# Performance work log

Measured on AMD Instinct MI355X. Metric: run time of the kernel, lower is better.

Reference implementation:

```python
import jax, jax.numpy as jnp
import numpy as np
import math

B, S, H, NH, K = 1, 4096, 1024, 16, 32
HD = H // NH


def setup_inputs() -> dict:
    key = jax.random.key(0)
    ks = jax.random.split(key, 8)
    x = jax.random.normal(ks[0], (B, S, H), dtype=jnp.float32)
    # per-query top-K indices; make them causal (idx[q] <= q) so every row has >=1 valid key
    idx_raw = jax.random.randint(ks[1], (S, K), 0, S)
    idx = idx_raw % (jnp.arange(S)[:, None] + 1)
    valid = jnp.ones((S, K), dtype=bool)
    geo_bias = jax.random.normal(ks[2], (NH, S, K), dtype=jnp.float32)
    scale = 1.0 / math.sqrt(H)
    Wq = jax.random.normal(ks[3], (H, H), dtype=jnp.float32) * scale
    Wk = jax.random.normal(ks[4], (H, H), dtype=jnp.float32) * scale
    Wv = jax.random.normal(ks[5], (H, H), dtype=jnp.float32) * scale
    Wo = jax.random.normal(ks[6], (H, H), dtype=jnp.float32) * scale
    bo = jnp.zeros((H,), dtype=jnp.float32)
    return {"x": x, "idx": idx, "valid": valid, "geo_bias": geo_bias,
            "Wq": Wq, "Wk": Wk, "Wv": Wv, "Wo": Wo, "bo": bo}


def reference(x, idx, valid, geo_bias, Wq, Wk, Wv, Wo, bo):
    b, s, h = x.shape
    nh = geo_bias.shape[0]
    hd = h // nh
    kk = idx.shape[1]
    # projections -> [b, nh, s, hd]
    def proj(W):
        return (x @ W).reshape(b, s, nh, hd).transpose(0, 2, 1, 3)
    q, k, v = proj(Wq), proj(Wk), proj(Wv)
    # gather per-query selected keys/values: [b, nh, s, K, hd]
    k_sel = k[:, :, idx]
    v_sel = v[:, :, idx]
    # scores via elementwise mult + reduce over head_dim
    logits = jnp.einsum('bhsd,bhskd->bhsk', q, k_sel) / math.sqrt(hd)
    logits = logits + geo_bias[None]
    mask = valid & (idx <= jnp.arange(s)[:, None])  # [s, K]
    logits = jnp.where(mask[None, None], logits, jnp.float32(-1e30))
    attn = jax.nn.softmax(logits, axis=-1)
    out = jnp.einsum('bhsk,bhskd->bhsd', attn, v_sel)
    out = out.transpose(0, 2, 1, 3).reshape(b, s, h)
    return out @ Wo + bo
```

## Files before the change

### kernel.cpp

```cpp
#include <hip/hip_runtime.h>
#include <hip/hip_bf16.h>
#include <stdint.h>

typedef unsigned short u16;
typedef __attribute__((ext_vector_type(8))) short bf16x8;
typedef __attribute__((ext_vector_type(4))) float f32x4;
typedef __attribute__((ext_vector_type(2))) float f32x2;

typedef const __attribute__((address_space(1))) unsigned int* gptr_t;
typedef __attribute__((address_space(3))) unsigned int* lptr_t;

__device__ __forceinline__ float bf2f(u16 v) {
    unsigned int u = ((unsigned int)v) << 16;
    float f;
    __builtin_memcpy(&f, &u, 4);
    return f;
}
__device__ __forceinline__ u16 f2bf(float f) {
    unsigned int u;
    __builtin_memcpy(&u, &f, 4);
    u += 0x7FFFu + ((u >> 16) & 1u);
    return (u16)(u >> 16);
}
__device__ __forceinline__ float bflo(unsigned int u) {
    unsigned int x = u << 16; float f; __builtin_memcpy(&f, &x, 4); return f;
}
__device__ __forceinline__ float bfhi(unsigned int u) {
    unsigned int x = u & 0xFFFF0000u; float f; __builtin_memcpy(&f, &x, 4); return f;
}
__device__ __forceinline__ f32x2 upk(unsigned int u) {
    return (f32x2){bflo(u), bfhi(u)};
}

#define BM 128
#define BN 128
#define BK 32

template <typename OUTT>
__global__ __launch_bounds__(256) void gemm_bt(const u16* __restrict__ A,
                                               const u16* __restrict__ Bt,
                                               OUTT* __restrict__ C,
                                               const float* __restrict__ bias,
                                               int M, int N, int K) {
    __shared__ u16 As[BM * BK];
    __shared__ u16 Bs[BN * BK];

    const int t    = threadIdx.x;
    const int lane = t & 63;
    const int wave = t >> 6;
    const int wm   = (wave >> 1) * 64;
    const int wn   = (wave & 1) * 64;
    const int m0   = blockIdx.y * BM;
    const int n0   = blockIdx.x * BN;

    const int row  = t >> 2;
    const int kcol = (t & 3) * 8;

    const int quad = lane >> 4;
    const int l16  = lane & 15;

    f32x4 acc[4][4];
#pragma unroll
    for (int i = 0; i < 4; i++)
#pragma unroll
        for (int j = 0; j < 4; j++) acc[i][j] = (f32x4){0.f, 0.f, 0.f, 0.f};

    for (int k0 = 0; k0 < K; k0 += BK) {
        const u16* ga  = A  + (size_t)(m0 + row) * K + k0 + kcol;
        const u16* ga2 = A  + (size_t)(m0 + 64 + row) * K + k0 + kcol;
        const u16* gb  = Bt + (size_t)(n0 + row) * K + k0 + kcol;
        const u16* gb2 = Bt + (size_t)(n0 + 64 + row) * K + k0 + kcol;
        __builtin_amdgcn_global_load_lds((gptr_t)ga,  (lptr_t)(&As[t * 8]),        16, 0, 0);
        __builtin_amdgcn_global_load_lds((gptr_t)ga2, (lptr_t)(&As[2048 + t * 8]), 16, 0, 0);
        __builtin_amdgcn_global_load_lds((gptr_t)gb,  (lptr_t)(&Bs[t * 8]),        16, 0, 0);
        __builtin_amdgcn_global_load_lds((gptr_t)gb2, (lptr_t)(&Bs[2048 + t * 8]), 16, 0, 0);
        __syncthreads();

        bf16x8 af[4], bfg[4];
#pragma unroll
        for (int i = 0; i < 4; i++)
            af[i] = *(const bf16x8*)&As[(wm + i * 16 + l16) * BK + quad * 8];
#pragma unroll
        for (int j = 0; j < 4; j++)
            bfg[j] = *(const bf16x8*)&Bs[(wn + j * 16 + l16) * BK + quad * 8];

#pragma unroll
        for (int i = 0; i < 4; i++)
#pragma unroll
            for (int j = 0; j < 4; j++)
                acc[i][j] = __builtin_amdgcn_mfma_f32_16x16x32_bf16(af[i], bfg[j], acc[i][j], 0, 0, 0);
        __syncthreads();
    }

#pragma unroll
    for (int j = 0; j < 4; j++) {
        const int n  = n0 + wn + j * 16 + l16;
        const float bv = bias ? bias[n] : 0.f;
#pragma unroll
        for (int i = 0; i < 4; i++) {
            const int mbase = m0 + wm + i * 16 + quad * 4;
#pragma unroll
            for (int r = 0; r < 4; r++) {
                const float v = acc[i][j][r] + bv;
                if constexpr (sizeof(OUTT) == 2)
                    C[(size_t)(mbase + r) * N + n] = (OUTT)f2bf(v);
                else
                    C[(size_t)(mbase + r) * N + n] = (OUTT)v;
            }
        }
    }
}

__global__ __launch_bounds__(512) void gemm_bt_w8(const u16* __restrict__ A,
                                                  const u16* __restrict__ Bt,
                                                  float* __restrict__ C,
                                                  const float* __restrict__ bias,
                                                  int M, int N, int K) {
    __shared__ u16 As[BM * BK];
    __shared__ u16 Bs[BN * BK];

    const int t    = threadIdx.x;
    const int lane = t & 63;
    const int wave = t >> 6;
    const int wm   = (wave >> 2) * 64;
    const int wn   = (wave & 3) * 32;
    const int m0   = blockIdx.y * BM;
    const int n0   = blockIdx.x * BN;

    const int row  = t >> 2;
    const int kcol = (t & 3) * 8;

    const int quad = lane >> 4;
    const int l16  = lane & 15;

    f32x4 acc[4][2];
#pragma unroll
    for (int i = 0; i < 4; i++)
#pragma unroll
        for (int j = 0; j < 2; j++) acc[i][j] = (f32x4){0.f, 0.f, 0.f, 0.f};

    for (int k0 = 0; k0 < K; k0 += BK) {
        const u16* ga = A  + (size_t)(m0 + row) * K + k0 + kcol;
        const u16* gb = Bt + (size_t)(n0 + row) * K + k0 + kcol;
        __builtin_amdgcn_global_load_lds((gptr_t)ga, (lptr_t)(&As[t * 8]), 16, 0, 0);
        __builtin_amdgcn_global_load_lds((gptr_t)gb, (lptr_t)(&Bs[t * 8]), 16, 0, 0);
        __syncthreads();

        bf16x8 af[4], bfg[2];
#pragma unroll
        for (int i = 0; i < 4; i++)
            af[i] = *(const bf16x8*)&As[(wm + i * 16 + l16) * BK + quad * 8];
#pragma unroll
        for (int j = 0; j < 2; j++)
            bfg[j] = *(const bf16x8*)&Bs[(wn + j * 16 + l16) * BK + quad * 8];

#pragma unroll
        for (int i = 0; i < 4; i++)
#pragma unroll
            for (int j = 0; j < 2; j++)
                acc[i][j] = __builtin_amdgcn_mfma_f32_16x16x32_bf16(af[i], bfg[j], acc[i][j], 0, 0, 0);
        __syncthreads();
    }

#pragma unroll
    for (int j = 0; j < 2; j++) {
        const int n  = n0 + wn + j * 16 + l16;
        const float bv = bias ? bias[n] : 0.f;
#pragma unroll
        for (int i = 0; i < 4; i++) {
            const int mbase = m0 + wm + i * 16 + quad * 4;
#pragma unroll
            for (int r = 0; r < 4; r++)
                C[(size_t)(mbase + r) * N + n] = acc[i][j][r] + bv;
        }
    }
}

__global__ __launch_bounds__(256) void prep_k(const float* __restrict__ x,
                                              const float* __restrict__ W0,
                                              const float* __restrict__ W1,
                                              const float* __restrict__ W2,
                                              const float* __restrict__ W3,
                                              u16* __restrict__ x_bf,
                                              u16* __restrict__ Dqkv,
                                              u16* __restrict__ Do) {
    const int b = blockIdx.x;
    if (b < 4096) {
        const int i = b * 256 + threadIdx.x;
        const float4 v = ((const float4*)x)[i];
        u16 o[4] = {f2bf(v.x), f2bf(v.y), f2bf(v.z), f2bf(v.w)};
        *(uint64_t*)&x_bf[i * 4] = *(uint64_t*)o;
        return;
    }
    __shared__ u16 tile[32][33];
    const int bb  = b - 4096;
    const int z   = bb >> 10;
    const int t10 = bb & 1023;
    const int c0  = (t10 & 31) * 32;
    const int r0  = (t10 >> 5) * 32;
    const float* src = (z == 0) ? W0 : (z == 1) ? W1 : (z == 2) ? W2 : W3;
    u16* dst = (z < 3) ? (Dqkv + (size_t)z * 1024 * 1024) : Do;
    const int tx = threadIdx.x & 31;
    const int ty = threadIdx.x >> 5;
#pragma unroll
    for (int i = 0; i < 32; i += 8)
        tile[ty + i][tx] = f2bf(src[(size_t)(r0 + ty + i) * 1024 + c0 + tx]);
    __syncthreads();
#pragma unroll
    for (int i = 0; i < 32; i += 8)
        dst[(size_t)(c0 + ty + i) * 1024 + r0 + tx] = tile[tx][ty + i];
}

__global__ __launch_bounds__(256, 8) void attn_k(const u16* __restrict__ QKV,
                                                 const int* __restrict__ idx,
                                                 const float* __restrict__ geo,
                                                 u16* __restrict__ AO) {
    __shared__ float dot_lds[4 * 64];
    __shared__ float w_lds[4 * 64];

    const int t    = threadIdx.x;
    const int lane = t & 63;
    const int wave = t >> 6;
    const int b    = blockIdx.x;
    const int hp   = b & 7;
    const int s    = ((b >> 3) << 2) + wave;
    const int h0   = hp * 2;
    const int hsel = lane >> 5;
    const int kk   = lane & 31;
    const int g    = lane >> 3;
    const int c8   = lane & 7;

    const char* qb = (const char*)QKV;

    const int j    = idx[s * 32 + kk];
    const int joff = j * 6144;

    const uint4 qA = *(const uint4*)(qb + (size_t)s * 6144 + h0 * 128 + c8 * 16);
    const uint4 qB = *(const uint4*)(qb + (size_t)s * 6144 + h0 * 128 + 128 + c8 * 16);
    const f32x2 qa0 = upk(qA.x), qa1 = upk(qA.y), qa2 = upk(qA.z), qa3 = upk(qA.w);
    const f32x2 qb0 = upk(qB.x), qb1 = upk(qB.y), qb2 = upk(qB.z), qb3 = upk(qB.w);

#pragma unroll
    for (int i = 0; i < 8; i++) {
        const int rh = i * 8 + g;
        const int jm = __shfl(j, rh & 31);
        const uint4 kv = *(const uint4*)(qb + (size_t)(unsigned)(jm * 6144) + 2048 +
                                         (h0 + (i >> 2)) * 128 + c8 * 16);
        f32x2 d2;
        if (i < 4) {
            d2  = upk(kv.x) * qa0;
            d2 += upk(kv.y) * qa1;
            d2 += upk(kv.z) * qa2;
            d2 += upk(kv.w) * qa3;
        } else {
            d2  = upk(kv.x) * qb0;
            d2 += upk(kv.y) * qb1;
            d2 += upk(kv.z) * qb2;
            d2 += upk(kv.w) * qb3;
        }
        float d = d2.x + d2.y;
        d += __shfl_xor(d, 1);
        d += __shfl_xor(d, 2);
        d += __shfl_xor(d, 4);
        if (c8 == 0) dot_lds[wave * 64 + rh] = d;
    }

    float lg2 = dot_lds[wave * 64 + lane] * 0.125f +
                geo[((size_t)(h0 + hsel) * 4096 + s) * 32 + kk];
    if (j > s) lg2 = -1e30f;

    float mx = lg2;
    mx = fmaxf(mx, __shfl_xor(mx, 16));
    mx = fmaxf(mx, __shfl_xor(mx, 8));
    mx = fmaxf(mx, __shfl_xor(mx, 4));
    mx = fmaxf(mx, __shfl_xor(mx, 2));
    mx = fmaxf(mx, __shfl_xor(mx, 1));
    const float p = __expf(lg2 - mx);
    float sum = p;
    sum += __shfl_xor(sum, 16);
    sum += __shfl_xor(sum, 8);
    sum += __shfl_xor(sum, 4);
    sum += __shfl_xor(sum, 2);
    sum += __shfl_xor(sum, 1);
    const float w = p / sum;
    w_lds[wave * 64 + lane] = w;

    const int vofs = 4096 + h0 * 128 + 4 * lane;
    f32x2 av = (f32x2){0.f, 0.f};
#pragma unroll
    for (int q = 0; q < 32; q++) {
        const int soff = __builtin_amdgcn_readlane(joff, q);
        const float wq = w_lds[wave * 64 + (lane & 32) + q];
        const unsigned int vv = *(const unsigned int*)(qb + (size_t)(unsigned)soff + vofs);
        av += wq * upk(vv);
    }
    const unsigned int packed = (unsigned int)f2bf(av.x) | ((unsigned int)f2bf(av.y) << 16);
    *(unsigned int*)&AO[(size_t)s * 1024 + h0 * 64 + 2 * lane] = packed;
}

extern "C" void kernel_launch(void* const* d_in, const int* in_sizes, int n_in,
                              void* d_out, int out_size, void* d_ws, size_t ws_size,
                              hipStream_t stream) {
    const float* x   = (const float*)d_in[0];
    const int*   idx = (const int*)d_in[1];
    const float* geo = (const float*)d_in[3];
    const float* Wq  = (const float*)d_in[4];
    const float* Wk  = (const float*)d_in[5];
    const float* Wv  = (const float*)d_in[6];
    const float* Wo  = (const float*)d_in[7];
    const float* bo  = (const float*)d_in[8];
    float* out = (float*)d_out;

    u16* x_bf   = (u16*)d_ws;
    u16* wt_qkv = x_bf + (size_t)4096 * 1024;
    u16* wt_o   = wt_qkv + (size_t)3 * 1024 * 1024;
    u16* qkv    = wt_o + (size_t)1024 * 1024;
    u16* ao     = qkv + (size_t)4096 * 3072;

    const dim3 tb(256);
    prep_k<<<dim3(8192), tb, 0, stream>>>(x, Wq, Wk, Wv, Wo, x_bf, wt_qkv, wt_o);

    gemm_bt<u16><<<dim3(3072 / BN, 4096 / BM), tb, 0, stream>>>(x_bf, wt_qkv, qkv, nullptr,
                                                                4096, 3072, 1024);
    attn_k<<<dim3(4096 * 8 / 4), tb, 0, stream>>>(qkv, idx, geo, ao);
    gemm_bt_w8<<<dim3(1024 / BN, 4096 / BM), dim3(512), 0, stream>>>(ao, wt_o, out, bo,
                                                                     4096, 1024, 1024);
}
```

Before: 188.3 us.

## Use BK=64 swizzled LDS tiles in QKV GEMM and widen attention V gather

The QKV projection GEMM now stages 64-wide K tiles in shared memory with an XOR swizzle on the 16-byte column chunks. This halves the number of barrier-separated iterations and is meant to avoid LDS bank conflicts on the fragment reads. Separately, the attention PV accumulation has each lane load 8 bytes (4 bf16) instead of 4, splits the 32 keys between the two half-waves, and combines the halves with a cross-half shuffle. The cost is more shared memory per block, which can lower occupancy, plus extra shuffles in attention.

```diff
diff --git a/kernel.cpp b/kernel.cpp
--- a/kernel.cpp
+++ b/kernel.cpp
@@ -36,14 +36,12 @@
 #define BN 128
 #define BK 32
 
-template <typename OUTT>
-__global__ __launch_bounds__(256) void gemm_bt(const u16* __restrict__ A,
-                                               const u16* __restrict__ Bt,
-                                               OUTT* __restrict__ C,
-                                               const float* __restrict__ bias,
-                                               int M, int N, int K) {
-    __shared__ u16 As[BM * BK];
-    __shared__ u16 Bs[BN * BK];
+__global__ __launch_bounds__(256) void gemm_bk64(const u16* __restrict__ A,
+                                                 const u16* __restrict__ Bt,
+                                                 u16* __restrict__ C,
+                                                 int M, int N, int K) {
+    __shared__ u16 As[BM * 64];
+    __shared__ u16 Bs[BN * 64];
 
     const int t    = threadIdx.x;
     const int lane = t & 63;
@@ -53,11 +51,13 @@
     const int m0   = blockIdx.y * BM;
     const int n0   = blockIdx.x * BN;
 
-    const int row  = t >> 2;
-    const int kcol = (t & 3) * 8;
+    const int r5   = t >> 3;
+    const int pc   = t & 7;
+    const int lc   = pc ^ (r5 & 7);
 
     const int quad = lane >> 4;
     const int l16  = lane & 15;
+    const int sw   = l16 & 7;
 
     f32x4 acc[4][4];
 #pragma unroll
@@ -65,48 +65,43 @@
 #pragma unroll
         for (int j = 0; j < 4; j++) acc[i][j] = (f32x4){0.f, 0.f, 0.f, 0.f};
 
-    for (int k0 = 0; k0 < K; k0 += BK) {
-        const u16* ga  = A  + (size_t)(m0 + row) * K + k0 + kcol;
-        const u16* ga2 = A  + (size_t)(m0 + 64 + row) * K + k0 + kcol;
-        const u16* gb  = Bt + (size_t)(n0 + row) * K + k0 + kcol;
-        const u16* gb2 = Bt + (size_t)(n0 + 64 + row) * K + k0 + kcol;
-        __builtin_amdgcn_global_load_lds((gptr_t)ga,  (lptr_t)(&As[t * 8]),        16, 0, 0);
-        __builtin_amdgcn_global_load_lds((gptr_t)ga2, (lptr_t)(&As[2048 + t * 8]), 16, 0, 0);
-        __builtin_amdgcn_global_load_lds((gptr_t)gb,  (lptr_t)(&Bs[t * 8]),        16, 0, 0);
-        __builtin_amdgcn_global_load_lds((gptr_t)gb2, (lptr_t)(&Bs[2048 + t * 8]), 16, 0, 0);
+    for (int k0 = 0; k0 < K; k0 += 64) {
+#pragma unroll
+        for (int p = 0; p < 4; p++) {
+            const u16* ga = A  + (size_t)(m0 + r5 + 32 * p) * K + k0 + lc * 8;
+            const u16* gb = Bt + (size_t)(n0 + r5 + 32 * p) * K + k0 + lc * 8;
+            __builtin_amdgcn_global_load_lds((gptr_t)ga, (lptr_t)(&As[t * 8 + p * 2048]), 16, 0, 0);
+            __builtin_amdgcn_global_load_lds((gptr_t)gb, (lptr_t)(&Bs[t * 8 + p * 2048]), 16, 0, 0);
+        }
         __syncthreads();
 
-        bf16x8 af[4], bfg[4];
-#pragma unroll
-        for (int i = 0; i < 4; i++)
-            af[i] = *(const bf16x8*)&As[(wm + i * 16 + l16) * BK + quad * 8];
-#pragma unroll
-        for (int j = 0; j < 4; j++)
-            bfg[j] = *(const bf16x8*)&Bs[(wn + j * 16 + l16) * BK + quad * 8];
-
-#pragma unroll
-        for (int i = 0; i < 4; i++)
+#pragma unroll
+        for (int k2 = 0; k2 < 2; k2++) {
+            bf16x8 af[4], bfg[4];
+#pragma unroll
+            for (int i = 0; i < 4; i++)
+                af[i] = *(const bf16x8*)&As[(wm + i * 16 + l16) * 64 + ((k2 * 4 + quad) ^ sw) * 8];
 #pragma unroll
             for (int j = 0; j < 4; j++)
-                acc[i][j] = __builtin_amdgcn_mfma_f32_16x16x32_bf16(af[i], bfg[j], acc[i][j], 0, 0, 0);
+                bfg[j] = *(const bf16x8*)&Bs[(wn + j * 16 + l16) * 64 + ((k2 * 4 + quad) ^ sw) * 8];
+#pragma unroll
+            for (int i = 0; i < 4; i++)
+#pragma unroll
+                for (int j = 0; j < 4; j++)
+                    acc[i][j] = __builtin_amdgcn_mfma_f32_16x16x32_bf16(af[i], bfg[j], acc[i][j], 0, 0, 0);
+        }
         __syncthreads();
     }
 
 #pragma unroll
     for (int j = 0; j < 4; j++) {
-        const int n  = n0 + wn + j * 16 + l16;
-        const float bv = bias ? bias[n] : 0.f;
+        const int n = n0 + wn + j * 16 + l16;
 #pragma unroll
         for (int i = 0; i < 4; i++) {
             const int mbase = m0 + wm + i * 16 + quad * 4;
 #pragma unroll
-            for (int r = 0; r < 4; r++) {
-                const float v = acc[i][j][r] + bv;
-                if constexpr (sizeof(OUTT) == 2)
-                    C[(size_t)(mbase + r) * N + n] = (OUTT)f2bf(v);
-                else
-                    C[(size_t)(mbase + r) * N + n] = (OUTT)v;
-            }
+            for (int r = 0; r < 4; r++)
+                C[(size_t)(mbase + r) * N + n] = f2bf(acc[i][j][r]);
         }
     }
 }
@@ -285,17 +280,30 @@
     const float w = p / sum;
     w_lds[wave * 64 + lane] = w;
 
-    const int vofs = 4096 + h0 * 128 + 4 * lane;
-    f32x2 av = (f32x2){0.f, 0.f};
-#pragma unroll
-    for (int q = 0; q < 32; q++) {
-        const int soff = __builtin_amdgcn_readlane(joff, q);
-        const float wq = w_lds[wave * 64 + (lane & 32) + q];
-        const unsigned int vv = *(const unsigned int*)(qb + (size_t)(unsigned)soff + vofs);
-        av += wq * upk(vv);
-    }
-    const unsigned int packed = (unsigned int)f2bf(av.x) | ((unsigned int)f2bf(av.y) << 16);
-    *(unsigned int*)&AO[(size_t)s * 1024 + h0 * 64 + 2 * lane] = packed;
+    const int half = lane >> 5;
+    const int e8   = lane & 31;
+    const int vconst = 4096 + h0 * 128 + 8 * e8;
+    const int whead  = (e8 >> 4) * 32;
+    f32x4 av = (f32x4){0.f, 0.f, 0.f, 0.f};
+#pragma unroll
+    for (int i = 0; i < 16; i++) {
+        const int   jo = __shfl(joff, 2 * i + half);
+        const float wq = w_lds[wave * 64 + whead + 2 * i + half];
+        const uint2 vv = *(const uint2*)(qb + (size_t)(unsigned)jo + vconst);
+        const f32x2 v01 = upk(vv.x), v23 = upk(vv.y);
+        av.x += wq * v01.x;
+        av.y += wq * v01.y;
+        av.z += wq * v23.x;
+        av.w += wq * v23.y;
+    }
+    av.x += __shfl_xor(av.x, 32);
+    av.y += __shfl_xor(av.y, 32);
+    av.z += __shfl_xor(av.z, 32);
+    av.w += __shfl_xor(av.w, 32);
+    if (lane < 32) {
+        u16 o[4] = {f2bf(av.x), f2bf(av.y), f2bf(av.z), f2bf(av.w)};
+        *(uint2*)&AO[(size_t)s * 1024 + h0 * 64 + 4 * lane] = *(uint2*)o;
+    }
 }
 
 extern "C" void kernel_launch(void* const* d_in, const int* in_sizes, int n_in,
@@ -320,9 +328,9 @@
     const dim3 tb(256);
     prep_k<<<dim3(8192), tb, 0, stream>>>(x, Wq, Wk, Wv, Wo, x_bf, wt_qkv, wt_o);
 
-    gemm_bt<u16><<<dim3(3072 / BN, 4096 / BM), tb, 0, stream>>>(x_bf, wt_qkv, qkv, nullptr,
-                                                                4096, 3072, 1024);
+    gemm_bk64<<<dim3(3072 / BN, 4096 / BM), tb, 0, stream>>>(
+        x_bf, wt_qkv, qkv, 4096, 3072, 1024);
     attn_k<<<dim3(4096 * 8 / 4), tb, 0, stream>>>(qkv, idx, geo, ao);
-    gemm_bt_w8<<<dim3(1024 / BN, 4096 / BM), dim3(512), 0, stream>>>(ao, wt_o, out, bo,
-                                                                     4096, 1024, 1024);
-}
+    gemm_bt_w8<<<dim3(1024 / BN, 4096 / BM), dim3(512), 0, stream>>>(
+        ao, wt_o, out, bo, 4096, 1024, 1024);
+}
```

New measurement: 184.7 us. No clear change (-1.9%).
